# Optimization experiments

Measured on AMD Instinct MI355X. Metric: run time of the kernel, lower is better.

## Reference

```python
import jax, jax.numpy as jnp
import numpy as np

B, N, M, K, QK, GEO = 2, 16384, 4096, 16, 64, 18
EPS = 1e-5


def _conv1d(x, w, b):  # x [B,C,N], w [O,C] -> [B,O,N]  (1x1 Conv1d)
    return jnp.einsum('oc,bcn->bon', w, x) + b[None, :, None]


def _bn1d(x, g, bt):  # train-mode BatchNorm1d: batch stats over (B, N)
    m = x.mean(axis=(0, 2), keepdims=True)
    v = x.var(axis=(0, 2), keepdims=True)
    return (x - m) * jax.lax.rsqrt(v + EPS) * g[None, :, None] + bt[None, :, None]


def _conv2d(x, w, b):  # x [B,C,N,K], w [O,C] -> [B,O,N,K]  (1x1 Conv2d)
    return jnp.einsum('oc,bcnk->bonk', w, x) + b[None, :, None, None]


def _bn2d(x, g, bt):
    m = x.mean(axis=(0, 2, 3), keepdims=True)
    v = x.var(axis=(0, 2, 3), keepdims=True)
    return (x - m) * jax.lax.rsqrt(v + EPS) * g[None, :, None, None] + bt[None, :, None, None]


def _gather(t, idx):  # t [B,C,M], idx [B,N,K] -> [B,C,N,K]; t_g[b,c,n,j] = t[b,c,idx[b,n,j]]
    return jnp.take_along_axis(t[:, :, None, :], idx[:, None, :, :], axis=3)


def setup_inputs() -> dict:
    key = jax.random.key(0)
    ks = iter(jax.random.split(key, 40))
    def rn(shape, s=0.02):
        return jax.random.normal(next(ks), shape, jnp.float32) * s
    def z(c):
        return jnp.zeros((c,), jnp.float32)
    def o(c):
        return jnp.ones((c,), jnp.float32)
    return dict(
        xyz_hr=jax.random.normal(next(ks), (B, 3, N), jnp.float32),
        xyz_lr=jax.random.normal(next(ks), (B, 3, M), jnp.float32),
        val_lr=jax.random.normal(next(ks), (B, 6, M), jnp.float32),
        feat_hr=jax.random.normal(next(ks), (B, GEO, N), jnp.float32),
        feat_lr=jax.random.normal(next(ks), (B, GEO, M), jnp.float32),
        ge_w1=rn((QK, GEO)), ge_b1=z(QK), ge_g1=o(QK), ge_bt1=z(QK),
        ge_w2=rn((QK, QK)), ge_b2=z(QK), ge_g2=o(QK), ge_bt2=z(QK),
        sc_w=rn((QK, 6)), sc_b=z(QK), sh_w=rn((QK, 6)), sh_b=z(QK),
        q_w=rn((QK, QK)), q_b=z(QK), k_w=rn((QK, QK)), k_b=z(QK),
        bh_w1=rn((32, QK)), bh_b1=z(32), bh_g=o(32), bh_bt=z(32),
        bh_w2=rn((1, 32)), bh_b2=z(1),
        rp_w1=rn((QK, 3)), rp_b1=z(QK), rp_g=o(QK), rp_bt=z(QK),
        rp_w2=rn((QK, QK)), rp_b2=z(QK),
    )


def reference(xyz_hr, xyz_lr, val_lr, feat_hr, feat_lr,
              ge_w1, ge_b1, ge_g1, ge_bt1, ge_w2, ge_b2, ge_g2, ge_bt2,
              sc_w, sc_b, sh_w, sh_b, q_w, q_b, k_w, k_b,
              bh_w1, bh_b1, bh_g, bh_bt, bh_w2, bh_b2,
              rp_w1, rp_b1, rp_g, rp_bt, rp_w2, rp_b2):
    def geom_enc(x):
        x = jax.nn.relu(_bn1d(_conv1d(x, ge_w1, ge_b1), ge_g1, ge_bt1))
        return jax.nn.relu(_bn1d(_conv1d(x, ge_w2, ge_b2), ge_g2, ge_bt2))

    geom_hr = geom_enc(feat_hr)   # [B,QK,N]
    geom_lr = geom_enc(feat_lr)   # [B,QK,M]

    # val_lr has 6 channels -> FiLM modulation branch is taken
    scale = _conv1d(val_lr, sc_w, sc_b)
    shift = _conv1d(val_lr, sh_w, sh_b)
    geom_lr = geom_lr * (scale + 1.0) + shift

    bdy = jax.nn.relu(_bn1d(_conv1d(geom_hr, bh_w1, bh_b1), bh_g, bh_bt))
    bdy_prob = jax.nn.sigmoid(_conv1d(bdy, bh_w2, bh_b2))  # [B,1,N]

    Q = _conv1d(geom_hr, q_w, q_b)   # [B,QK,N]
    Kf = _conv1d(geom_lr, k_w, k_b)  # [B,QK,M]

    # kNN under no_grad: squared euclidean via expansion (same ordering as cdist)
    a = xyz_hr.transpose(0, 2, 1)  # [B,N,3]
    b = xyz_lr.transpose(0, 2, 1)  # [B,M,3]
    d2 = (jnp.sum(a * a, -1)[:, :, None] + jnp.sum(b * b, -1)[:, None, :]
          - 2.0 * jnp.einsum('bnc,bmc->bnm', a, b))
    d2 = jax.lax.stop_gradient(d2)
    _, idx = jax.lax.top_k(-d2, K)  # [B,N,K] indices of K nearest low-res points

    K_g = _gather(Kf, idx)            # [B,QK,N,K]
    xyz_lr_g = _gather(xyz_lr, idx)   # [B,3,N,K]
    rel_pos = xyz_hr[:, :, :, None] - xyz_lr_g
    pe = jax.nn.relu(_bn2d(_conv2d(rel_pos, rp_w1, rp_b1), rp_g, rp_bt))
    pos_enc = _conv2d(pe, rp_w2, rp_b2)  # [B,QK,N,K]

    scores = jnp.einsum('bcn,bcnk->bnk', Q, K_g + pos_enc) / jnp.sqrt(jnp.float32(QK))
    attn = jax.nn.softmax(scores, axis=-1)          # [B,N,K]
    val_g = _gather(val_lr, idx)                    # [B,6,N,K]
    out = jnp.einsum('bnk,bcnk->bcn', attn, val_g)  # [B,6,N]
    return out, bdy_prob
```

## Files before the change

### kernel.cpp

```cpp
#include <hip/hip_runtime.h>

#define BB 2
#define NN 16384
#define MM 4096
#define KK 16
#define CQ 64
#define GEOC 18
#define EPSV 1e-5
#define SPL 8

__device__ __forceinline__ float dist2f(float sa, float ax, float ay, float az, float4 p) {
#pragma clang fp contract(off)
  return (sa + p.w) - 2.0f * ((ax * p.x + ay * p.y) + az * p.z);
}

__device__ __forceinline__ void ce(float& a, float& b) {
  float lo = fminf(a, b), hi = fmaxf(a, b); a = lo; b = hi;
}
__device__ __forceinline__ void sort8(float* v) {
  ce(v[0],v[1]); ce(v[2],v[3]); ce(v[4],v[5]); ce(v[6],v[7]);
  ce(v[0],v[2]); ce(v[1],v[3]); ce(v[4],v[6]); ce(v[5],v[7]);
  ce(v[1],v[2]); ce(v[5],v[6]);
  ce(v[0],v[4]); ce(v[1],v[5]); ce(v[2],v[6]); ce(v[3],v[7]);
  ce(v[2],v[4]); ce(v[3],v[5]);
  ce(v[1],v[2]); ce(v[3],v[4]); ce(v[5],v[6]);
}
__device__ __forceinline__ void bitonic16(float* v) {
#pragma unroll
  for (int i = 0; i < 8; i++) ce(v[i], v[i + 8]);
  ce(v[0],v[4]); ce(v[1],v[5]); ce(v[2],v[6]); ce(v[3],v[7]);
  ce(v[8],v[12]); ce(v[9],v[13]); ce(v[10],v[14]); ce(v[11],v[15]);
  ce(v[0],v[2]); ce(v[1],v[3]); ce(v[4],v[6]); ce(v[5],v[7]);
  ce(v[8],v[10]); ce(v[9],v[11]); ce(v[12],v[14]); ce(v[13],v[15]);
  ce(v[0],v[1]); ce(v[2],v[3]); ce(v[4],v[5]); ce(v[6],v[7]);
  ce(v[8],v[9]); ce(v[10],v[11]); ce(v[12],v[13]); ce(v[14],v[15]);
}
__device__ __forceinline__ void merge16_8(float* dv, const float* t) {
  dv[8]  = fminf(dv[8],  t[7]);  dv[9]  = fminf(dv[9],  t[6]);
  dv[10] = fminf(dv[10], t[5]);  dv[11] = fminf(dv[11], t[4]);
  dv[12] = fminf(dv[12], t[3]);  dv[13] = fminf(dv[13], t[2]);
  dv[14] = fminf(dv[14], t[1]);  dv[15] = fminf(dv[15], t[0]);
  bitonic16(dv);
}

__global__ __launch_bounds__(256) void init_k(const float* __restrict__ xyz,
    const float* __restrict__ val, float* __restrict__ xyzT, float* __restrict__ valT,
    const float* __restrict__ qw, const float* __restrict__ qb, const float* __restrict__ w2,
    float* __restrict__ R, float* __restrict__ rb, int* __restrict__ hdr)
{
#pragma clang fp contract(off)
  if (blockIdx.x < 32) {
    int i = blockIdx.x * 256 + threadIdx.x;
    int b = i / MM, m = i % MM;
    float x = xyz[(b * 3 + 0) * MM + m];
    float y = xyz[(b * 3 + 1) * MM + m];
    float z = xyz[(b * 3 + 2) * MM + m];
    float sb = (x * x + y * y) + z * z;
    ((float4*)xyzT)[i] = make_float4(x, y, z, sb);
    float v0 = val[((size_t)b * 6 + 0) * MM + m];
    float v1 = val[((size_t)b * 6 + 1) * MM + m];
    float v2 = val[((size_t)b * 6 + 2) * MM + m];
    float v3 = val[((size_t)b * 6 + 3) * MM + m];
    float v4 = val[((size_t)b * 6 + 4) * MM + m];
    float v5 = val[((size_t)b * 6 + 5) * MM + m];
    ((float4*)valT)[2 * i]     = make_float4(v0, v1, v2, v3);
    ((float4*)valT)[2 * i + 1] = make_float4(v4, v5, 0.f, 0.f);
  } else {
    int t = threadIdx.x;
    for (int wd = t; wd < 1376; wd += 256) hdr[wd] = 0;
#pragma unroll
    for (int e = t * 16; e < t * 16 + 16; e++) {
      int o = e >> 6, i = e & 63;
      float acc = 0.f;
#pragma unroll
      for (int p = 0; p < CQ; p++) acc = fmaf(w2[p * CQ + o], qw[p * CQ + i], acc);
      R[e] = acc;
    }
    if (t < CQ) {
      float a = 0.f;
#pragma unroll
      for (int p = 0; p < CQ; p++) a = fmaf(w2[p * CQ + t], qb[p], a);
      rb[t] = a;
    }
  }
}

template<int CIN, int COUT, int OBLK, bool TOUT>
__device__ __forceinline__ void conv_body(int tid, const float* __restrict__ x,
    const float* __restrict__ W, const float* __restrict__ bias,
    const float* __restrict__ AB, float* __restrict__ y, int L)
{
  int g = tid / (BB * L);
  int i = tid % (BB * L);
  int b = i / L, n = i % L;
  const float* xp = x + (size_t)b * CIN * L + n;
  float xr[CIN];
#pragma unroll
  for (int c = 0; c < CIN; c++) {
    float v = xp[(size_t)c * L];
    if (AB) v = fmaxf(fmaf(v, AB[c], AB[CIN + c]), 0.f);
    xr[c] = v;
  }
#pragma unroll
  for (int oo = 0; oo < OBLK; oo++) {
    int o = g * OBLK + oo;
    float acc = bias ? bias[o] : 0.f;
#pragma unroll
    for (int c = 0; c < CIN; c++)
      acc = fmaf(W[(size_t)o * CIN + c], xr[c], acc);
    if (TOUT) y[((size_t)b * L + n) * COUT + o] = acc;
    else      y[((size_t)b * COUT + o) * L + n] = acc;
  }
}

template<int CIN, int COUT, int OBLK, bool TOUT>
__global__ __launch_bounds__(256) void conv_k(const float* __restrict__ x,
    const float* __restrict__ W, const float* __restrict__ bias,
    const float* __restrict__ AB, float* __restrict__ y, int L)
{
  conv_body<CIN, COUT, OBLK, TOUT>(blockIdx.x * 256 + threadIdx.x, x, W, bias, AB, y, L);
}

template<int CIN, int COUT, int OBLK>
__global__ __launch_bounds__(256) void convhl_k(const float* __restrict__ xh,
    const float* __restrict__ xl, const float* __restrict__ W, const float* __restrict__ bias,
    const float* __restrict__ ABh, const float* __restrict__ ABl,
    float* __restrict__ yh, float* __restrict__ yl, int hb)
{
  if ((int)blockIdx.x < hb)
    conv_body<CIN, COUT, OBLK, false>(blockIdx.x * 256 + threadIdx.x, xh, W, bias, ABh, yh, NN);
  else
    conv_body<CIN, COUT, OBLK, false>((blockIdx.x - hb) * 256 + threadIdx.x, xl, W, bias, ABl, yl, MM);
}

template<int C, int NCH>
__device__ __forceinline__ void stats_body(int bid, const float* __restrict__ t, int L,
    const float* __restrict__ g, const float* __restrict__ bt,
    double* __restrict__ sums, int* __restrict__ counter, float* __restrict__ AB)
{
  int c = bid % C;
  int ch = bid / C;
  const size_t tot = (size_t)BB * L;
  const size_t slab = tot / NCH;
  size_t beg = slab * ch, end = beg + slab;
  double s = 0.0, ss = 0.0;
  for (size_t idx = beg + threadIdx.x; idx < end; idx += 256) {
    int b = (int)(idx / L); int i = (int)(idx % L);
    double v = t[((size_t)b * C + c) * L + i];
    s += v; ss += v * v;
  }
  for (int o = 32; o >= 1; o >>= 1) { s += __shfl_down(s, o); ss += __shfl_down(ss, o); }
  __shared__ double sh[8];
  __shared__ int lastf;
  int w = threadIdx.x >> 6;
  if ((threadIdx.x & 63) == 0) { sh[2 * w] = s; sh[2 * w + 1] = ss; }
  __syncthreads();
  if (threadIdx.x == 0) {
    for (int j = 1; j < 4; j++) { s += sh[2 * j]; ss += sh[2 * j + 1]; }
    atomicAdd(&sums[c], s);
    atomicAdd(&sums[C + c], ss);
    __threadfence();
    int old = atomicAdd(counter, 1);
    lastf = (old == C * NCH - 1) ? 1 : 0;
  }
  __syncthreads();
  if (lastf && threadIdx.x < C) {
    __threadfence();
    int cc = threadIdx.x;
    double S  = atomicAdd(&sums[cc], 0.0);
    double SS = atomicAdd(&sums[C + cc], 0.0);
    double nn = (double)BB * L;
    double mean = S / nn, var = SS / nn - mean * mean;
    double A = (double)g[cc] / sqrt(var + EPSV);
    AB[cc] = (float)A;
    AB[C + cc] = (float)((double)bt[cc] - mean * A);
  }
}

template<int C, int NCH>
__global__ __launch_bounds__(256) void statsone_k(const float* __restrict__ t, int L,
    const float* __restrict__ g, const float* __restrict__ bt,
    double* __restrict__ sums, int* __restrict__ counter, float* __restrict__ AB)
{
  stats_body<C, NCH>(blockIdx.x, t, L, g, bt, sums, counter, AB);
}

template<int C, int NCH>
__global__ __launch_bounds__(256) void statshl_k(const float* __restrict__ t0, int L0,
    const float* __restrict__ t1, int L1, const float* __restrict__ g,
    const float* __restrict__ bt, double* __restrict__ sums, int* __restrict__ ctrs,
    float* __restrict__ AB0, float* __restrict__ AB1)
{
  if ((int)blockIdx.x < C * NCH)
    stats_body<C, NCH>(blockIdx.x, t0, L0, g, bt, sums, ctrs, AB0);
  else
    stats_body<C, NCH>(blockIdx.x - C * NCH, t1, L1, g, bt, sums + 2 * C, ctrs + 1, AB1);
}

__global__ __launch_bounds__(256) void fk_k(const float* __restrict__ t2l,
    const float* __restrict__ ABl, const float* __restrict__ val,
    const float* __restrict__ scw, const float* __restrict__ scb,
    const float* __restrict__ shw, const float* __restrict__ shb,
    const float* __restrict__ kw, const float* __restrict__ kb,
    float* __restrict__ KfT)
{
  int tid = blockIdx.x * 256 + threadIdx.x;
  int g = tid & 7;
  int i = tid >> 3;
  int b = i / MM, m = i % MM;
  float v6[6];
#pragma unroll
  for (int j = 0; j < 6; j++) v6[j] = val[((size_t)b * 6 + j) * MM + m];
  float xr[CQ];
#pragma unroll
  for (int c = 0; c < CQ; c++) {
    float gv = fmaxf(fmaf(t2l[((size_t)b * CQ + c) * MM + m], ABl[c], ABl[CQ + c]), 0.f);
    float sc = scb[c], sh = shb[c];
#pragma unroll
    for (int j = 0; j < 6; j++) {
      sc = fmaf(scw[c * 6 + j], v6[j], sc);
      sh = fmaf(shw[c * 6 + j], v6[j], sh);
    }
    xr[c] = fmaf(gv, 1.f + sc, sh);
  }
#pragma unroll
  for (int oo = 0; oo < 8; oo++) {
    int o = g * 8 + oo;
    float acc = kb[o];
#pragma unroll
    for (int c = 0; c < CQ; c++) acc = fmaf(kw[o * CQ + c], xr[c], acc);
    KfT[(size_t)i * CQ + o] = acc;
  }
}

__global__ __launch_bounds__(256) void convqq_k(const float* __restrict__ x,
    const float* __restrict__ Wq, const float* __restrict__ bq,
    const float* __restrict__ R, const float* __restrict__ rb,
    const float* __restrict__ AB, float* __restrict__ Q, float* __restrict__ Qp)
{
  int tid = blockIdx.x * 256 + threadIdx.x;
  int g = tid / (BB * NN);
  int i = tid % (BB * NN);
  int b = i / NN, n = i % NN;
  const float* xp = x + (size_t)b * CQ * NN + n;
  float xr[CQ];
#pragma unroll
  for (int c = 0; c < CQ; c++)
    xr[c] = fmaxf(fmaf(xp[(size_t)c * NN], AB[c], AB[CQ + c]), 0.f);
#pragma unroll
  for (int oo = 0; oo < 16; oo++) {
    int o = g * 16 + oo;
    float aq = bq[o], ap = rb[o];
#pragma unroll
    for (int c = 0; c < CQ; c++) {
      aq = fmaf(Wq[o * CQ + c], xr[c], aq);
      ap = fmaf(R[o * CQ + c], xr[c], ap);
    }
    Q[((size_t)b * CQ + o) * NN + n] = aq;
    Qp[((size_t)b * CQ + o) * NN + n] = ap;
  }
}

__global__ __launch_bounds__(256) void bdy_k(const float* __restrict__ tb,
    const float* __restrict__ AB, const float* __restrict__ w2,
    const float* __restrict__ b2, float* __restrict__ out2)
{
  int i = blockIdx.x * 256 + threadIdx.x;
  int b = i / NN, n = i % NN;
  float acc = b2[0];
#pragma unroll
  for (int c = 0; c < 32; c++) {
    float v = tb[((size_t)b * 32 + c) * NN + n];
    v = fmaxf(fmaf(v, AB[c], AB[32 + c]), 0.f);
    acc = fmaf(w2[c], v, acc);
  }
  out2[i] = 1.f / (1.f + expf(-acc));
}

__global__ __launch_bounds__(256) void knnA_k(const float* __restrict__ xyz_hr,
    const float* __restrict__ xyzT, float* __restrict__ theta)
{
#pragma clang fp contract(off)
  int tid = blockIdx.x * 256 + threadIdx.x;
  int s = tid & (SPL - 1);
  int qi = tid / SPL;
  int b = qi / NN, n = qi % NN;
  float ax = xyz_hr[(b * 3 + 0) * NN + n];
  float ay = xyz_hr[(b * 3 + 1) * NN + n];
  float az = xyz_hr[(b * 3 + 2) * NN + n];
  float sa = (ax * ax + ay * ay) + az * az;
  const float4* __restrict__ Ps = ((const float4*)xyzT) + (size_t)b * MM + s;
  float dv[16];
#pragma unroll
  for (int j = 0; j < 16; j++) dv[j] = 3.4e38f;
  for (int j = 0; j < MM / SPL; j += 8) {
    float t[8];
#pragma unroll
    for (int u = 0; u < 8; u++) {
      float4 p = Ps[(size_t)(j + u) * SPL];
      t[u] = dist2f(sa, ax, ay, az, p);
    }
    sort8(t);
    merge16_8(dv, t);
  }
#pragma unroll
  for (int mask = 1; mask <= 4; mask <<= 1) {
    float c[16];
#pragma unroll
    for (int j = 0; j < 16; j++) c[j] = __shfl_xor(dv[15 - j], mask);
#pragma unroll
    for (int j = 0; j < 16; j++) dv[j] = fminf(dv[j], c[j]);
    bitonic16(dv);
  }
  if (s == 0) theta[qi] = dv[15];
}

__global__ __launch_bounds__(256) void knnC_k(const float* __restrict__ xyz_hr,
    const float* __restrict__ xyzT, const float* __restrict__ theta,
    int* __restrict__ idx_out, double* __restrict__ mompart)
{
#pragma clang fp contract(off)
  __shared__ int s_clt[4], s_ceq[4];
  __shared__ int s_lt[4][16];
  __shared__ int s_eq[4][64];
  __shared__ int s_sel[4][16];
  __shared__ float s_mom[4][9];
  int w = threadIdx.x >> 6, l = threadIdx.x & 63;
  int qi = blockIdx.x * 4 + w;
  int b = qi / NN, n = qi % NN;
  if (l == 0) { s_clt[w] = 0; s_ceq[w] = 0; }
  __syncthreads();
  float ax = xyz_hr[(b * 3 + 0) * NN + n];
  float ay = xyz_hr[(b * 3 + 1) * NN + n];
  float az = xyz_hr[(b * 3 + 2) * NN + n];
  float sa = (ax * ax + ay * ay) + az * az;
  float th = theta[qi];
  const float4* __restrict__ P = ((const float4*)xyzT) + (size_t)b * MM;
  for (int j = 0; j < MM / 64; j++) {
    int m = j * 64 + l;
    float d = dist2f(sa, ax, ay, az, P[m]);
    if (d < th) {
      int pos = atomicAdd(&s_clt[w], 1);
      if (pos < 16) s_lt[w][pos] = m;
    } else if (d == th) {
      int pos = atomicAdd(&s_ceq[w], 1);
      if (pos < 64) s_eq[w][pos] = m;
    }
  }
  __syncthreads();
  if (l == 0) {
    int clt = s_clt[w]; if (clt > 16) clt = 16;
    int ceq = s_ceq[w]; if (ceq > 64) ceq = 64;
    for (int j = 0; j < clt; j++) s_sel[w][j] = s_lt[w][j];
    int need = KK - clt;
    for (int t = 0; t < need; t++) {
      int best = 0x7fffffff, bp = 0;
      for (int j = 0; j < ceq; j++) { int v = s_eq[w][j]; if (v < best) { best = v; bp = j; } }
      s_sel[w][clt + t] = best;
      s_eq[w][bp] = 0x7fffffff;
    }
    size_t base = (size_t)qi * KK;
    for (int j = 0; j < KK; j++) idx_out[base + j] = s_sel[w][j];
  }
  __syncthreads();
  float t9[9];
#pragma unroll
  for (int j = 0; j < 9; j++) t9[j] = 0.f;
  if (l < 16) {
    float4 p = P[s_sel[w][l]];
    float rx = ax - p.x, ry = ay - p.y, rz = az - p.z;
    t9[0] = rx; t9[1] = ry; t9[2] = rz;
    t9[3] = rx * rx; t9[4] = ry * ry; t9[5] = rz * rz;
    t9[6] = rx * ry; t9[7] = rx * rz; t9[8] = ry * rz;
  }
#pragma unroll
  for (int j = 0; j < 9; j++)
    for (int o = 32; o >= 1; o >>= 1) t9[j] += __shfl_down(t9[j], o);
  if (l == 0) { for (int j = 0; j < 9; j++) s_mom[w][j] = t9[j]; }
  __syncthreads();
  if (threadIdx.x == 0) {
    double* op = mompart + (size_t)blockIdx.x * 9;
    for (int j = 0; j < 9; j++)
      op[j] = (double)s_mom[0][j] + (double)s_mom[1][j] + (double)s_mom[2][j] + (double)s_mom[3][j];
  }
}

__global__ __launch_bounds__(256) void mom2_k(const double* __restrict__ part, int nblk,
    const float* __restrict__ w1, const float* __restrict__ b1,
    const float* __restrict__ g, const float* __restrict__ bt, float* __restrict__ AB)
{
  double acc[9];
#pragma unroll
  for (int j = 0; j < 9; j++) acc[j] = 0.0;
  for (int blk = threadIdx.x; blk < nblk; blk += 256) {
    const double* p = part + (size_t)blk * 9;
#pragma unroll
    for (int j = 0; j < 9; j++) acc[j] += p[j];
  }
#pragma unroll
  for (int j = 0; j < 9; j++)
    for (int o = 32; o >= 1; o >>= 1) acc[j] += __shfl_down(acc[j], o);
  __shared__ double sh[4][9];
  __shared__ double mo[9];
  int w = threadIdx.x >> 6, l = threadIdx.x & 63;
  if (l == 0) { for (int j = 0; j < 9; j++) sh[w][j] = acc[j]; }
  __syncthreads();
  if (threadIdx.x == 0) {
    for (int wv = 1; wv < 4; wv++) for (int j = 0; j < 9; j++) sh[0][j] += sh[wv][j];
    for (int j = 0; j < 9; j++) mo[j] = sh[0][j];
  }
  __syncthreads();
  if (threadIdx.x < CQ) {
    int c = threadIdx.x;
    double cnt = (double)BB * NN * KK;
    double mx = mo[0]/cnt, my = mo[1]/cnt, mz = mo[2]/cnt;
    double cxx = mo[3]/cnt - mx*mx, cyy = mo[4]/cnt - my*my, czz = mo[5]/cnt - mz*mz;
    double cxy = mo[6]/cnt - mx*my, cxz = mo[7]/cnt - mx*mz, cyz = mo[8]/cnt - my*mz;
    double wx = w1[c*3], wy = w1[c*3+1], wz = w1[c*3+2];
    double mean = wx*mx + wy*my + wz*mz + (double)b1[c];
    double var = wx*wx*cxx + wy*wy*cyy + wz*wz*czz + 2.0*(wx*wy*cxy + wx*wz*cxz + wy*wz*cyz);
    double A = (double)g[c] / sqrt(var + EPSV);
    AB[c] = (float)A;
    AB[CQ + c] = (float)((double)bt[c] - mean * A);
  }
}

__global__ __launch_bounds__(256) void attn_k(
    const float* __restrict__ Q, const float* __restrict__ Qp,
    const float* __restrict__ KfT, const int* __restrict__ idxb,
    const float* __restrict__ xyzT, const float* __restrict__ valT,
    const float* __restrict__ xyz_hr, const float* __restrict__ AB,
    const float* __restrict__ w1, const float* __restrict__ b1,
    const float* __restrict__ b2, float* __restrict__ out)
{
  __shared__ float q_s[CQ * 16], qp_s[CQ * 16];
  const int ngrp = NN / 16;
  int b = blockIdx.x / ngrp;
  int n0 = (blockIdx.x % ngrp) * 16;
  for (int t = threadIdx.x; t < CQ * 16; t += 256) {
    int c = t >> 4, j = t & 15;
    q_s[t]  = Q [((size_t)b * CQ + c) * NN + n0 + j];
    qp_s[t] = Qp[((size_t)b * CQ + c) * NN + n0 + j];
  }
  __syncthreads();
  int q = threadIdx.x >> 4, k = threadIdx.x & 15;
  int n = n0 + q;
  int id = idxb[((size_t)b * NN + n) * KK + k];
  float ax = xyz_hr[(b * 3 + 0) * NN + n];
  float ay = xyz_hr[(b * 3 + 1) * NN + n];
  float az = xyz_hr[(b * 3 + 2) * NN + n];
  float4 pl = ((const float4*)xyzT)[(size_t)b * MM + id];
  float rx = ax - pl.x, ry = ay - pl.y, rz = az - pl.z;
  const float4* kg = (const float4*)(KfT + ((size_t)b * MM + id) * CQ);
  float s = 0.f;
#pragma unroll
  for (int c4 = 0; c4 < CQ / 4; c4++) {
    float4 g4 = kg[c4];
    float ga[4] = {g4.x, g4.y, g4.z, g4.w};
#pragma unroll
    for (int u = 0; u < 4; u++) {
      int c = 4 * c4 + u;
      float t0 = fmaf(w1[c * 3 + 0], rx, fmaf(w1[c * 3 + 1], ry, w1[c * 3 + 2] * rz)) + b1[c];
      float pe = fmaxf(fmaf(t0, AB[c], AB[CQ + c]), 0.f);
      s = fmaf(q_s[c * 16 + q], ga[u] + b2[c], s);
      s = fmaf(qp_s[c * 16 + q], pe, s);
    }
  }
  s *= 0.125f;
  float mx = s;
#pragma unroll
  for (int o = 8; o >= 1; o >>= 1) mx = fmaxf(mx, __shfl_xor(mx, o, 16));
  float p = expf(s - mx);
  float sum = p;
#pragma unroll
  for (int o = 8; o >= 1; o >>= 1) sum += __shfl_xor(sum, o, 16);
  float attn = p / sum;
  const float4* vt = (const float4*)(valT + ((size_t)b * MM + id) * 8);
  float4 va = vt[0], vb = vt[1];
  float oc[6] = {attn*va.x, attn*va.y, attn*va.z, attn*va.w, attn*vb.x, attn*vb.y};
#pragma unroll
  for (int c = 0; c < 6; c++) {
    float a = oc[c];
#pragma unroll
    for (int o = 8; o >= 1; o >>= 1) a += __shfl_xor(a, o, 16);
    oc[c] = a;
  }
  if (k == 0) {
#pragma unroll
    for (int c = 0; c < 6; c++) out[((size_t)b * 6 + c) * NN + n] = oc[c];
  }
}

extern "C" void kernel_launch(void* const* d_in, const int* in_sizes, int n_in,
                              void* d_out, int out_size, void* d_ws, size_t ws_size,
                              hipStream_t stream)
{
  const float* xyz_hr = (const float*)d_in[0];
  const float* xyz_lr = (const float*)d_in[1];
  const float* val_lr = (const float*)d_in[2];
  const float* feat_hr= (const float*)d_in[3];
  const float* feat_lr= (const float*)d_in[4];
  const float* ge_w1 = (const float*)d_in[5];
  const float* ge_b1 = (const float*)d_in[6];
  const float* ge_g1 = (const float*)d_in[7];
  const float* ge_bt1= (const float*)d_in[8];
  const float* ge_w2 = (const float*)d_in[9];
  const float* ge_b2 = (const float*)d_in[10];
  const float* ge_g2 = (const float*)d_in[11];
  const float* ge_bt2= (const float*)d_in[12];
  const float* sc_w = (const float*)d_in[13];
  const float* sc_b = (const float*)d_in[14];
  const float* sh_w = (const float*)d_in[15];
  const float* sh_b = (const float*)d_in[16];
  const float* q_w  = (const float*)d_in[17];
  const float* q_b  = (const float*)d_in[18];
  const float* k_w  = (const float*)d_in[19];
  const float* k_b  = (const float*)d_in[20];
  const float* bh_w1= (const float*)d_in[21];
  const float* bh_b1= (const float*)d_in[22];
  const float* bh_g = (const float*)d_in[23];
  const float* bh_bt= (const float*)d_in[24];
  const float* bh_w2= (const float*)d_in[25];
  const float* bh_b2= (const float*)d_in[26];
  const float* rp_w1= (const float*)d_in[27];
  const float* rp_b1= (const float*)d_in[28];
  const float* rp_g = (const float*)d_in[29];
  const float* rp_bt= (const float*)d_in[30];
  const float* rp_w2= (const float*)d_in[31];
  const float* rp_b2= (const float*)d_in[32];
  float* out = (float*)d_out;

  int*    hdr  = (int*)d_ws;
  int*    ctrs = (int*)((char*)d_ws + 96);
  double* sums = (double*)((char*)d_ws + 128);
  float*  base = (float*)((char*)d_ws + 5504);
  float* AB1h = base;
  float* AB2h = base + 128;
  float* AB1l = base + 256;
  float* AB2l = base + 384;
  float* ABb  = base + 512;
  float* AB2d = base + 576;
  float* big  = base + 768;
  float* t1_hr = big;
  float* t2_hr = t1_hr + 2097152;
  float* Qb    = t2_hr + 2097152;
  float* Qp    = Qb    + 2097152;
  float* t1_lr = Qp    + 2097152;
  float* t2_lr = t1_lr + 524288;
  float* Rbuf  = t2_lr + 524288;
  float* KfT   = Rbuf  + 524288;
  float* tb    = KfT   + 524288;
  float* xyzT  = tb    + 1048576;
  float* valT  = xyzT  + 32768;
  int*   idxb  = (int*)(valT + 65536);
  float* theta = Qb;
  double* mompart = (double*)Qp;
  float* Rw    = Rbuf;
  float* rbv   = Rbuf + 4096;

  init_k<<<33, 256, 0, stream>>>(xyz_lr, val_lr, xyzT, valT, q_w, q_b, rp_w2, Rw, rbv, hdr);

  knnA_k<<<(BB * NN * SPL) / 256, 256, 0, stream>>>(xyz_hr, xyzT, theta);
  knnC_k<<<(BB * NN) / 4, 256, 0, stream>>>(xyz_hr, xyzT, theta, idxb, mompart);
  mom2_k<<<1, 256, 0, stream>>>(mompart, (BB * NN) / 4, rp_w1, rp_b1, rp_g, rp_bt, AB2d);

  convhl_k<GEOC, CQ, 16><<<640, 256, 0, stream>>>(feat_hr, feat_lr, ge_w1, ge_b1,
                                                  nullptr, nullptr, t1_hr, t1_lr, 512);
  statshl_k<CQ, 8><<<1024, 256, 0, stream>>>(t1_hr, NN, t1_lr, MM, ge_g1, ge_bt1,
                                             sums, ctrs + 0, AB1h, AB1l);
  convhl_k<CQ, CQ, 16><<<640, 256, 0, stream>>>(t1_hr, t1_lr, ge_w2, ge_b2,
                                                AB1h, AB1l, t2_hr, t2_lr, 512);
  statshl_k<CQ, 8><<<1024, 256, 0, stream>>>(t2_hr, NN, t2_lr, MM, ge_g2, ge_bt2,
                                             sums + 256, ctrs + 2, AB2h, AB2l);

  fk_k<<<256, 256, 0, stream>>>(t2_lr, AB2l, val_lr, sc_w, sc_b, sh_w, sh_b,
                                k_w, k_b, KfT);

  conv_k<CQ, 32, 16, false><<<256, 256, 0, stream>>>(t2_hr, bh_w1, bh_b1, AB2h, tb, NN);
  statsone_k<32, 8><<<256, 256, 0, stream>>>(tb, NN, bh_g, bh_bt, sums + 512, ctrs + 4, ABb);
  bdy_k<<<128, 256, 0, stream>>>(tb, ABb, bh_w2, bh_b2, out + (size_t)BB * 6 * NN);

  convqq_k<<<512, 256, 0, stream>>>(t2_hr, q_w, q_b, Rw, rbv, AB2h, Qb, Qp);

  attn_k<<<2048, 256, 0, stream>>>(Qb, Qp, KfT, idxb, xyzT, valT, xyz_hr, AB2d,
                                   rp_w1, rp_b1, rp_b2, out);
}
```

Baseline: 570.6 us.

## Batch 8 queries per wave in kNN select, fuse head convs and bdy into attn

The kNN threshold-select kernel now has each wave handle 8 query points instead of 1. Each loaded low-res point is reused across 8 distance computations, which cuts global loads and the number of blocks by 8x, and the moment reduction is adjusted to match. The boundary-head conv is merged with the Q/Qp conv into one launch, and the final boundary sigmoid is folded into extra blocks of the attention kernel, removing two launches. The cost is more registers and shared-memory atomics per wave, plus a larger shared footprint.

```diff
diff --git a/kernel.cpp b/kernel.cpp
--- a/kernel.cpp
+++ b/kernel.cpp
@@ -113,14 +113,6 @@
   }
 }
 
-template<int CIN, int COUT, int OBLK, bool TOUT>
-__global__ __launch_bounds__(256) void conv_k(const float* __restrict__ x,
-    const float* __restrict__ W, const float* __restrict__ bias,
-    const float* __restrict__ AB, float* __restrict__ y, int L)
-{
-  conv_body<CIN, COUT, OBLK, TOUT>(blockIdx.x * 256 + threadIdx.x, x, W, bias, AB, y, L);
-}
-
 template<int CIN, int COUT, int OBLK>
 __global__ __launch_bounds__(256) void convhl_k(const float* __restrict__ xh,
     const float* __restrict__ xl, const float* __restrict__ W, const float* __restrict__ bias,
@@ -233,10 +225,12 @@
   }
 }
 
-__global__ __launch_bounds__(256) void convqq_k(const float* __restrict__ x,
+__global__ __launch_bounds__(256) void convbqq_k(const float* __restrict__ x,
+    const float* __restrict__ bw, const float* __restrict__ bb,
     const float* __restrict__ Wq, const float* __restrict__ bq,
     const float* __restrict__ R, const float* __restrict__ rb,
-    const float* __restrict__ AB, float* __restrict__ Q, float* __restrict__ Qp)
+    const float* __restrict__ AB, float* __restrict__ tb,
+    float* __restrict__ Q, float* __restrict__ Qp)
 {
   int tid = blockIdx.x * 256 + threadIdx.x;
   int g = tid / (BB * NN);
@@ -247,34 +241,19 @@
 #pragma unroll
   for (int c = 0; c < CQ; c++)
     xr[c] = fmaxf(fmaf(xp[(size_t)c * NN], AB[c], AB[CQ + c]), 0.f);
+  const float* W; const float* bias; float* y; int o0;
+  if (g < 2)      { W = bw; bias = bb; y = tb; o0 = g * 16;       }
+  else if (g < 6) { W = Wq; bias = bq; y = Q;  o0 = (g - 2) * 16; }
+  else            { W = R;  bias = rb; y = Qp; o0 = (g - 6) * 16; }
+  int COUTL = (g < 2) ? 32 : CQ;
 #pragma unroll
   for (int oo = 0; oo < 16; oo++) {
-    int o = g * 16 + oo;
-    float aq = bq[o], ap = rb[o];
-#pragma unroll
-    for (int c = 0; c < CQ; c++) {
-      aq = fmaf(Wq[o * CQ + c], xr[c], aq);
-      ap = fmaf(R[o * CQ + c], xr[c], ap);
-    }
-    Q[((size_t)b * CQ + o) * NN + n] = aq;
-    Qp[((size_t)b * CQ + o) * NN + n] = ap;
-  }
-}
-
-__global__ __launch_bounds__(256) void bdy_k(const float* __restrict__ tb,
-    const float* __restrict__ AB, const float* __restrict__ w2,
-    const float* __restrict__ b2, float* __restrict__ out2)
-{
-  int i = blockIdx.x * 256 + threadIdx.x;
-  int b = i / NN, n = i % NN;
-  float acc = b2[0];
-#pragma unroll
-  for (int c = 0; c < 32; c++) {
-    float v = tb[((size_t)b * 32 + c) * NN + n];
-    v = fmaxf(fmaf(v, AB[c], AB[32 + c]), 0.f);
-    acc = fmaf(w2[c], v, acc);
-  }
-  out2[i] = 1.f / (1.f + expf(-acc));
+    int o = o0 + oo;
+    float acc = bias[o];
+#pragma unroll
+    for (int c = 0; c < CQ; c++) acc = fmaf(W[o * CQ + c], xr[c], acc);
+    y[((size_t)b * COUTL + o) * NN + n] = acc;
+  }
 }
 
 __global__ __launch_bounds__(256) void knnA_k(const float* __restrict__ xyz_hr,
@@ -320,58 +299,74 @@
     int* __restrict__ idx_out, double* __restrict__ mompart)
 {
 #pragma clang fp contract(off)
-  __shared__ int s_clt[4], s_ceq[4];
-  __shared__ int s_lt[4][16];
-  __shared__ int s_eq[4][64];
-  __shared__ int s_sel[4][16];
+  __shared__ int s_clt[32], s_ceq[32];
+  __shared__ int s_lt[32][16];
+  __shared__ int s_eq[32][64];
+  __shared__ int s_sel[32][16];
   __shared__ float s_mom[4][9];
   int w = threadIdx.x >> 6, l = threadIdx.x & 63;
-  int qi = blockIdx.x * 4 + w;
-  int b = qi / NN, n = qi % NN;
-  if (l == 0) { s_clt[w] = 0; s_ceq[w] = 0; }
-  __syncthreads();
-  float ax = xyz_hr[(b * 3 + 0) * NN + n];
-  float ay = xyz_hr[(b * 3 + 1) * NN + n];
-  float az = xyz_hr[(b * 3 + 2) * NN + n];
-  float sa = (ax * ax + ay * ay) + az * az;
-  float th = theta[qi];
+  int qblk = blockIdx.x * 32;
+  int b = qblk / NN;
+  int n0 = qblk % NN + w * 8;
+  if (threadIdx.x < 32) { s_clt[threadIdx.x] = 0; s_ceq[threadIdx.x] = 0; }
+  __syncthreads();
+  float qx[8], qy[8], qz[8], qs[8], th[8];
+#pragma unroll
+  for (int q = 0; q < 8; q++) {
+    qx[q] = xyz_hr[(b * 3 + 0) * NN + n0 + q];
+    qy[q] = xyz_hr[(b * 3 + 1) * NN + n0 + q];
+    qz[q] = xyz_hr[(b * 3 + 2) * NN + n0 + q];
+    qs[q] = (qx[q] * qx[q] + qy[q] * qy[q]) + qz[q] * qz[q];
+    th[q] = theta[(size_t)b * NN + n0 + q];
+  }
   const float4* __restrict__ P = ((const float4*)xyzT) + (size_t)b * MM;
   for (int j = 0; j < MM / 64; j++) {
     int m = j * 64 + l;
-    float d = dist2f(sa, ax, ay, az, P[m]);
-    if (d < th) {
-      int pos = atomicAdd(&s_clt[w], 1);
-      if (pos < 16) s_lt[w][pos] = m;
-    } else if (d == th) {
-      int pos = atomicAdd(&s_ceq[w], 1);
-      if (pos < 64) s_eq[w][pos] = m;
-    }
-  }
-  __syncthreads();
-  if (l == 0) {
-    int clt = s_clt[w]; if (clt > 16) clt = 16;
-    int ceq = s_ceq[w]; if (ceq > 64) ceq = 64;
-    for (int j = 0; j < clt; j++) s_sel[w][j] = s_lt[w][j];
+    float4 p = P[m];
+#pragma unroll
+    for (int q = 0; q < 8; q++) {
+      float d = (qs[q] + p.w) - 2.0f * ((qx[q] * p.x + qy[q] * p.y) + qz[q] * p.z);
+      int qq = w * 8 + q;
+      if (d < th[q]) {
+        int pos = atomicAdd(&s_clt[qq], 1);
+        if (pos < 16) s_lt[qq][pos] = m;
+      } else if (d == th[q]) {
+        int pos = atomicAdd(&s_ceq[qq], 1);
+        if (pos < 64) s_eq[qq][pos] = m;
+      }
+    }
+  }
+  __syncthreads();
+  if (threadIdx.x < 32) {
+    int qq = threadIdx.x;
+    int clt = s_clt[qq]; if (clt > 16) clt = 16;
+    int ceq = s_ceq[qq]; if (ceq > 64) ceq = 64;
+    for (int j = 0; j < clt; j++) s_sel[qq][j] = s_lt[qq][j];
     int need = KK - clt;
     for (int t = 0; t < need; t++) {
       int best = 0x7fffffff, bp = 0;
-      for (int j = 0; j < ceq; j++) { int v = s_eq[w][j]; if (v < best) { best = v; bp = j; } }
-      s_sel[w][clt + t] = best;
-      s_eq[w][bp] = 0x7fffffff;
-    }
-    size_t base = (size_t)qi * KK;
-    for (int j = 0; j < KK; j++) idx_out[base + j] = s_sel[w][j];
+      for (int j = 0; j < ceq; j++) { int v = s_eq[qq][j]; if (v < best) { best = v; bp = j; } }
+      s_sel[qq][clt + t] = best;
+      s_eq[qq][bp] = 0x7fffffff;
+    }
+    size_t base = ((size_t)qblk + qq) * KK;
+    for (int j = 0; j < KK; j++) idx_out[base + j] = s_sel[qq][j];
   }
   __syncthreads();
   float t9[9];
 #pragma unroll
   for (int j = 0; j < 9; j++) t9[j] = 0.f;
-  if (l < 16) {
-    float4 p = P[s_sel[w][l]];
+  for (int slot = threadIdx.x; slot < 512; slot += 256) {
+    int qq = slot >> 4, jj = slot & 15;
+    int nn_ = qblk % NN + qq;
+    float ax = xyz_hr[(b * 3 + 0) * NN + nn_];
+    float ay = xyz_hr[(b * 3 + 1) * NN + nn_];
+    float az = xyz_hr[(b * 3 + 2) * NN + nn_];
+    float4 p = P[s_sel[qq][jj]];
     float rx = ax - p.x, ry = ay - p.y, rz = az - p.z;
-    t9[0] = rx; t9[1] = ry; t9[2] = rz;
-    t9[3] = rx * rx; t9[4] = ry * ry; t9[5] = rz * rz;
-    t9[6] = rx * ry; t9[7] = rx * rz; t9[8] = ry * rz;
+    t9[0] += rx; t9[1] += ry; t9[2] += rz;
+    t9[3] += rx * rx; t9[4] += ry * ry; t9[5] += rz * rz;
+    t9[6] += rx * ry; t9[7] += rx * rz; t9[8] += ry * rz;
   }
 #pragma unroll
   for (int j = 0; j < 9; j++)
@@ -431,9 +426,24 @@
     const float* __restrict__ xyzT, const float* __restrict__ valT,
     const float* __restrict__ xyz_hr, const float* __restrict__ AB,
     const float* __restrict__ w1, const float* __restrict__ b1,
-    const float* __restrict__ b2, float* __restrict__ out)
+    const float* __restrict__ b2, float* __restrict__ out,
+    const float* __restrict__ tb, const float* __restrict__ ABb,
+    const float* __restrict__ bhw2, const float* __restrict__ bhb2)
 {
   __shared__ float q_s[CQ * 16], qp_s[CQ * 16];
+  if (blockIdx.x >= 2048) {
+    int i = (blockIdx.x - 2048) * 256 + threadIdx.x;
+    int b = i / NN, n = i % NN;
+    float acc = bhb2[0];
+#pragma unroll
+    for (int c = 0; c < 32; c++) {
+      float v = tb[((size_t)b * 32 + c) * NN + n];
+      v = fmaxf(fmaf(v, ABb[c], ABb[32 + c]), 0.f);
+      acc = fmaf(bhw2[c], v, acc);
+    }
+    out[(size_t)BB * 6 * NN + i] = 1.f / (1.f + expf(-acc));
+    return;
+  }
   const int ngrp = NN / 16;
   int b = blockIdx.x / ngrp;
   int n0 = (blockIdx.x % ngrp) * 16;
@@ -561,8 +571,8 @@
   init_k<<<33, 256, 0, stream>>>(xyz_lr, val_lr, xyzT, valT, q_w, q_b, rp_w2, Rw, rbv, hdr);
 
   knnA_k<<<(BB * NN * SPL) / 256, 256, 0, stream>>>(xyz_hr, xyzT, theta);
-  knnC_k<<<(BB * NN) / 4, 256, 0, stream>>>(xyz_hr, xyzT, theta, idxb, mompart);
-  mom2_k<<<1, 256, 0, stream>>>(mompart, (BB * NN) / 4, rp_w1, rp_b1, rp_g, rp_bt, AB2d);
+  knnC_k<<<(BB * NN) / 32, 256, 0, stream>>>(xyz_hr, xyzT, theta, idxb, mompart);
+  mom2_k<<<1, 256, 0, stream>>>(mompart, (BB * NN) / 32, rp_w1, rp_b1, rp_g, rp_bt, AB2d);
 
   convhl_k<GEOC, CQ, 16><<<640, 256, 0, stream>>>(feat_hr, feat_lr, ge_w1, ge_b1,
                                                   nullptr, nullptr, t1_hr, t1_lr, 512);
@@ -576,12 +586,10 @@
   fk_k<<<256, 256, 0, stream>>>(t2_lr, AB2l, val_lr, sc_w, sc_b, sh_w, sh_b,
                                 k_w, k_b, KfT);
 
-  conv_k<CQ, 32, 16, false><<<256, 256, 0, stream>>>(t2_hr, bh_w1, bh_b1, AB2h, tb, NN);
+  convbqq_k<<<1280, 256, 0, stream>>>(t2_hr, bh_w1, bh_b1, q_w, q_b, Rw, rbv,
+                                      AB2h, tb, Qb, Qp);
   statsone_k<32, 8><<<256, 256, 0, stream>>>(tb, NN, bh_g, bh_bt, sums + 512, ctrs + 4, ABb);
-  bdy_k<<<128, 256, 0, stream>>>(tb, ABb, bh_w2, bh_b2, out + (size_t)BB * 6 * NN);
-
-  convqq_k<<<512, 256, 0, stream>>>(t2_hr, q_w, q_b, Rw, rbv, AB2h, Qb, Qp);
-
-  attn_k<<<2048, 256, 0, stream>>>(Qb, Qp, KfT, idxb, xyzT, valT, xyz_hr, AB2d,
-                                   rp_w1, rp_b1, rp_b2, out);
-}
+
+  attn_k<<<2048 + 128, 256, 0, stream>>>(Qb, Qp, KfT, idxb, xyzT, valT, xyz_hr, AB2d,
+                                         rp_w1, rp_b1, rp_b2, out, tb, ABb, bh_w2, bh_b2);
+}
```

Result: faster. 530.9 us (-7.0%).
